# Kernel tuning notes

Measured on AMD Instinct MI355X. Metric: run time of the kernel, lower is better.

The kernel has to match this reference:

```python
import jax, jax.numpy as jnp
import numpy as np

B, S, D, H, W = 2, 4096, 1024, 8, 1024  # batch, seq, model_dim, heads, window
DH = D // H
EPS = 1e-5


def setup_inputs() -> dict:
    key = jax.random.key(0)
    ks = jax.random.split(key, 4)
    scale = 0.02
    return {
        "val": jax.random.normal(ks[0], (B, S, D), dtype=jnp.float32),
        "w_qkv": jax.random.normal(ks[1], (D, 3 * D), dtype=jnp.float32) * scale,
        "b_qkv": jnp.zeros((3 * D,), dtype=jnp.float32),
        "w_out": jax.random.normal(ks[2], (D, D), dtype=jnp.float32) * scale,
        "b_out": jnp.zeros((D,), dtype=jnp.float32),
        "ln_gamma": jnp.ones((D,), dtype=jnp.float32),
        "ln_beta": jnp.zeros((D,), dtype=jnp.float32),
    }


def _layer_norm(x, gamma, beta):
    mu = jnp.mean(x, axis=-1, keepdims=True)
    var = jnp.mean(jnp.square(x - mu), axis=-1, keepdims=True)
    return (x - mu) * jax.lax.rsqrt(var + EPS) * gamma + beta


def reference(val, w_qkv, b_qkv, w_out, b_out, ln_gamma, ln_beta):
    nb = S // W  # number of local windows
    qkv = val @ w_qkv + b_qkv                       # [B, S, 3D]
    qkv = qkv.reshape(B, nb, W, 3, H, DH)
    q, k, v = qkv[..., 0, :, :], qkv[..., 1, :, :], qkv[..., 2, :, :]  # [B,nb,W,H,DH]
    scores = jnp.einsum("bnwhd,bnxhd->bnhwx", q, k) / jnp.sqrt(jnp.float32(DH))
    attn = jax.nn.softmax(scores, axis=-1)          # [B,nb,H,W,W]
    ctx = jnp.einsum("bnhwx,bnxhd->bnwhd", attn, v).reshape(B, S, D)
    attn_out = ctx @ w_out + b_out                  # [B,S,D]
    return _layer_norm(val + attn_out, ln_gamma, ln_beta)
```

## Files before the change

### kernel.cpp

```cpp
#include <hip/hip_runtime.h>
#include <hip/hip_bf16.h>
#include <stdint.h>


typedef float f32x4 __attribute__((ext_vector_type(4)));
typedef __bf16 bf16x8 __attribute__((ext_vector_type(8)));

static __device__ __forceinline__ unsigned short f2bf(float f) {
    unsigned int u = __builtin_bit_cast(unsigned int, f);
    u += 0x7fffu + ((u >> 16) & 1u);
    return (unsigned short)(u >> 16);
}

static __device__ __forceinline__ unsigned cvt_pk_bf16(float lo, float hi) {
    unsigned r;
    asm("v_cvt_pk_bf16_f32 %0, %1, %2" : "=v"(r) : "v"(lo), "v"(hi));
    return r;
}

static __device__ __forceinline__ void gload_lds16(const void* g, void* l) {
    __builtin_amdgcn_global_load_lds(
        (__attribute__((address_space(1))) void*)(g),
        (__attribute__((address_space(3))) void*)(l), 16, 0, 0);
}

#define VMCNT(n) asm volatile("s_waitcnt vmcnt(" #n ")" ::: "memory")
#define SB() __builtin_amdgcn_sched_barrier(0)

__global__ __launch_bounds__(256) void k_convert(const float* __restrict__ in,
                                                 unsigned short* __restrict__ out,
                                                 int n4) {
    int i = blockIdx.x * 256 + threadIdx.x;
    if (i >= n4) return;
    float4 v = ((const float4*)in)[i];
    ushort4 o;
    o.x = f2bf(v.x); o.y = f2bf(v.y); o.z = f2bf(v.z); o.w = f2bf(v.w);
    ((ushort4*)out)[i] = o;
}

__global__ __launch_bounds__(256) void k_transpose(const float* __restrict__ in,
                                                   unsigned short* __restrict__ out,
                                                   int R, int C) {
    __shared__ float tile[64][65];
    const int rt = blockIdx.y * 64, ct = blockIdx.x * 64;
    const int t = threadIdx.x;
#pragma unroll
    for (int i = 0; i < 4; ++i) {
        int fid = i * 256 + t;
        int r = fid >> 4;
        int c = (fid & 15) << 2;
        float4 v = *(const float4*)&in[(size_t)(rt + r) * C + ct + c];
        tile[r][c] = v.x; tile[r][c + 1] = v.y; tile[r][c + 2] = v.z; tile[r][c + 3] = v.w;
    }
    __syncthreads();
#pragma unroll
    for (int i = 0; i < 4; ++i) {
        int fid = i * 256 + t;
        int c = fid >> 4;
        int r0 = (fid & 15) << 2;
        ushort4 o;
        o.x = f2bf(tile[r0][c]);     o.y = f2bf(tile[r0 + 1][c]);
        o.z = f2bf(tile[r0 + 2][c]); o.w = f2bf(tile[r0 + 3][c]);
        *(ushort4*)&out[(size_t)(ct + c) * R + rt + r0] = o;
    }
}

template <int MODE, int NTILES>
__global__ __launch_bounds__(512) void k_gemm(
    const unsigned short* __restrict__ A,
    const unsigned short* __restrict__ Bt,
    const float* __restrict__ bias,
    const float* __restrict__ resid,
    unsigned short* __restrict__ out_qk,
    unsigned short* __restrict__ out_vT,
    float* __restrict__ out_f)
{
    __shared__ __align__(16) char smem[147456];
    const int t = threadIdx.x;
    const int wave = t >> 6, lane = t & 63;
    const int lr = lane & 15, lg = lane >> 4;
    const int wr = wave >> 1, wc = wave & 1;

    const int lid = blockIdx.x;
    const int swz = (lid & 7) * (4 * NTILES) + (lid >> 3);
    const int tile_m = (swz / NTILES) * 256;
    const int tile_n = (swz % NTILES) * 128;

    const int srow = lane >> 3;
    const int sblk = (lane & 7) ^ srow;

    f32x4 acc[4][4];
#pragma unroll
    for (int i = 0; i < 4; ++i)
#pragma unroll
        for (int j = 0; j < 4; ++j)
            acc[i][j] = (f32x4){0.f, 0.f, 0.f, 0.f};

    auto stage2 = [&](int kt, int buf, int h) {
#pragma unroll
        for (int i = 0; i < 2; ++i) {
            int r = h * 128 + i * 64 + wave * 8 + srow;
            int dst = buf * 49152 + h * 16384 + i * 8192 + wave * 1024 + lane * 16;
            gload_lds16(&A[(size_t)(tile_m + r) * 1024 + kt * 64 + sblk * 8], smem + dst);
        }
        int rb = h * 64 + wave * 8 + srow;
        int dstb = buf * 49152 + 32768 + h * 8192 + wave * 1024 + lane * 16;
        gload_lds16(&Bt[(size_t)(tile_n + rb) * 1024 + kt * 64 + sblk * 8], smem + dstb);
    };

    stage2(0, 0, 0); stage2(0, 0, 1);
    stage2(1, 1, 0); stage2(1, 1, 1);

    bf16x8 af[4][2], bf[2][2];

    for (int kt = 0; kt < 16; ++kt) {
        const int buf = kt % 3;
        if (kt == 15) { VMCNT(0); } else { VMCNT(6); }
        SB(); __builtin_amdgcn_s_barrier(); SB();

        const int abase = buf * 49152;
        const int bbase = buf * 49152 + 32768;

#pragma unroll
        for (int mi = 0; mi < 4; ++mi) {
            const int row = wr * 64 + mi * 16 + lr;
#pragma unroll
            for (int kk = 0; kk < 2; ++kk)
                af[mi][kk] = *(const bf16x8*)(smem + abase + row * 128 +
                                (((kk * 4 + lg) ^ (row & 7)) << 4));
        }
#pragma unroll
        for (int ni = 0; ni < 2; ++ni) {
            const int row = wc * 64 + ni * 16 + lr;
#pragma unroll
            for (int kk = 0; kk < 2; ++kk)
                bf[ni][kk] = *(const bf16x8*)(smem + bbase + row * 128 +
                                (((kk * 4 + lg) ^ (row & 7)) << 4));
        }
        if (kt < 14) stage2(kt + 2, (kt + 2) % 3, 0);

        __builtin_amdgcn_s_setprio(1);
#pragma unroll
        for (int kk = 0; kk < 2; ++kk)
#pragma unroll
            for (int mi = 0; mi < 4; ++mi)
#pragma unroll
                for (int ni = 0; ni < 2; ++ni)
                    acc[mi][ni] = __builtin_amdgcn_mfma_f32_16x16x32_bf16(
                        af[mi][kk], bf[ni][kk], acc[mi][ni], 0, 0, 0);
        __builtin_amdgcn_s_setprio(0);

#pragma unroll
        for (int ni = 0; ni < 2; ++ni) {
            const int row = wc * 64 + 32 + ni * 16 + lr;
#pragma unroll
            for (int kk = 0; kk < 2; ++kk)
                bf[ni][kk] = *(const bf16x8*)(smem + bbase + row * 128 +
                                (((kk * 4 + lg) ^ (row & 7)) << 4));
        }
        if (kt < 14) stage2(kt + 2, (kt + 2) % 3, 1);

        __builtin_amdgcn_s_setprio(1);
#pragma unroll
        for (int kk = 0; kk < 2; ++kk)
#pragma unroll
            for (int mi = 0; mi < 4; ++mi)
#pragma unroll
                for (int ni = 0; ni < 2; ++ni)
                    acc[mi][2 + ni] = __builtin_amdgcn_mfma_f32_16x16x32_bf16(
                        af[mi][kk], bf[ni][kk], acc[mi][2 + ni], 0, 0, 0);
        __builtin_amdgcn_s_setprio(0);
    }

#pragma unroll
    for (int J = 0; J < 4; ++J) {
        const int n = tile_n + wc * 64 + J * 16 + lr;
        const float bv = bias[n];
#pragma unroll
        for (int I = 0; I < 4; ++I) {
            const int m0 = tile_m + wr * 64 + I * 16 + lg * 4;
            f32x4 v = acc[I][J];
            if (MODE == 0) {
                if (n < 2048) {
#pragma unroll
                    for (int r = 0; r < 4; ++r)
                        out_qk[(size_t)(m0 + r) * 2048 + n] = f2bf(v[r] + bv);
                } else {
                    int hd = (n - 2048) >> 7;
                    int dd = (n - 2048) & 127;
                    int bn = m0 >> 10;
                    int x0 = m0 & 1023;
                    ushort4 o;
                    o.x = f2bf(v[0] + bv); o.y = f2bf(v[1] + bv);
                    o.z = f2bf(v[2] + bv); o.w = f2bf(v[3] + bv);
                    *(ushort4*)&out_vT[((size_t)(bn * 8 + hd) * 128 + dd) * 1024 + x0] = o;
                }
            } else {
#pragma unroll
                for (int r = 0; r < 4; ++r) {
                    size_t idx = (size_t)(m0 + r) * 1024 + n;
                    out_f[idx] = v[r] + bv + resid[idx];
                }
            }
        }
    }
}

__global__ __launch_bounds__(256, 2) void k_attn(
    const unsigned short* __restrict__ qk,
    const unsigned short* __restrict__ vT,
    unsigned short* __restrict__ ctx)
{
    __shared__ __align__(16) unsigned short Kl[2 * 64 * 128];
    __shared__ __align__(16) unsigned short Vl[2 * 128 * 64];
    __shared__ __align__(16) unsigned short Pl[128 * 64];
    const int t = threadIdx.x;
    const int wave = t >> 6, lane = t & 63;
    const int lr = lane & 15, lg = lane >> 4;

    const int lid = blockIdx.y * gridDim.x + blockIdx.x;
    const int xcd = lid & 7, slot = lid >> 3;
    const int head = xcd * 8 + (slot & 7);
    const int qblk = slot >> 3;

    const int h = head & 7;
    const int tok0 = (head >> 3) * 1024;
    const int qtok = tok0 + qblk * 128 + wave * 32;
    const float cl2 = 0.08838834764831845f * 1.44269504088896f;

    const unsigned short* kbase = &qk[(size_t)tok0 * 2048 + 1024 + h * 128];
    const unsigned short* vhead = &vT[(size_t)head * 128 * 1024];

    auto stage = [&](int x0, int buf) {
        unsigned short* Kb = (unsigned short*)((char*)Kl + buf * 16384);
        unsigned short* Vb = (unsigned short*)((char*)Vl + buf * 16384);
#pragma unroll
        for (int i = 0; i < 4; ++i) {
            int x = i * 16 + wave * 4 + (lane >> 4);
            int ck = (lane & 15) ^ (x & 7);
            gload_lds16(&kbase[(size_t)(x0 + x) * 2048 + ck * 8], &Kb[i * 2048 + wave * 512]);
            int d = i * 32 + wave * 8 + (lane >> 3);
            int cv = (lane & 7) ^ (d & 7);
            gload_lds16(&vhead[(size_t)d * 1024 + x0 + cv * 8], &Vb[i * 2048 + wave * 512]);
        }
    };

    bf16x8 qf[2][4];
#pragma unroll
    for (int nq = 0; nq < 2; ++nq)
#pragma unroll
        for (int kk = 0; kk < 4; ++kk)
            qf[nq][kk] = *(const bf16x8*)&qk[(size_t)(qtok + 16 * nq + lr) * 2048 + h * 128 + kk * 32 + lg * 8];

    f32x4 o[2][8];
#pragma unroll
    for (int a = 0; a < 2; ++a)
#pragma unroll
        for (int b = 0; b < 8; ++b)
            o[a][b] = (f32x4){0.f, 0.f, 0.f, 0.f};
    float m_run[2] = {-3.0e38f, -3.0e38f};
    float l_run[2] = {0.f, 0.f};

    stage(0, 0);

    for (int tile = 0; tile < 16; ++tile) {
        const int kb = (tile & 1) * 16384;
        if (tile < 15) {
            stage((tile + 1) * 64, (tile + 1) & 1);
            VMCNT(8);
        } else {
            VMCNT(0);
        }
        SB(); __builtin_amdgcn_s_barrier(); SB();

        f32x4 s[4][2];
#pragma unroll
        for (int mi = 0; mi < 4; ++mi)
#pragma unroll
            for (int nq = 0; nq < 2; ++nq)
                s[mi][nq] = (f32x4){0.f, 0.f, 0.f, 0.f};
#pragma unroll
        for (int kk = 0; kk < 4; ++kk) {
            bf16x8 kf[4];
#pragma unroll
            for (int mi = 0; mi < 4; ++mi) {
                int row = mi * 16 + lr;
                int byte = (row * 256 + kk * 64 + lg * 16) ^ ((row & 7) << 4);
                kf[mi] = *(const bf16x8*)((const char*)Kl + kb + byte);
            }
            __builtin_amdgcn_s_setprio(1);
#pragma unroll
            for (int mi = 0; mi < 4; ++mi)
#pragma unroll
                for (int nq = 0; nq < 2; ++nq)
                    s[mi][nq] = __builtin_amdgcn_mfma_f32_16x16x32_bf16(kf[mi], qf[nq][kk], s[mi][nq], 0, 0, 0);
            __builtin_amdgcn_s_setprio(0);
        }

        float fac[2];
        bool doresc[2];
#pragma unroll
        for (int nq = 0; nq < 2; ++nq) {
            float mx = -3.0e38f;
#pragma unroll
            for (int mi = 0; mi < 4; ++mi)
#pragma unroll
                for (int r = 0; r < 4; ++r)
                    mx = fmaxf(mx, s[mi][nq][r]);
            mx = fmaxf(mx, __shfl_xor(mx, 16));
            mx = fmaxf(mx, __shfl_xor(mx, 32));
            float mxl = mx * cl2;
            float mr = m_run[nq];
            if (__any(mxl - mr > 8.0f)) {
                float mn = fmaxf(mr, mxl);
                fac[nq] = __builtin_amdgcn_exp2f(mr - mn);
                m_run[nq] = mn;
                doresc[nq] = true;
            } else {
                fac[nq] = 1.0f;
                doresc[nq] = false;
            }
            const float nmn = -m_run[nq];
            float sum = 0.f;
            const int q = wave * 32 + nq * 16 + lr;
#pragma unroll
            for (int mi = 0; mi < 4; ++mi) {
                float p0 = __builtin_amdgcn_exp2f(__builtin_fmaf(s[mi][nq][0], cl2, nmn));
                float p1 = __builtin_amdgcn_exp2f(__builtin_fmaf(s[mi][nq][1], cl2, nmn));
                float p2 = __builtin_amdgcn_exp2f(__builtin_fmaf(s[mi][nq][2], cl2, nmn));
                float p3 = __builtin_amdgcn_exp2f(__builtin_fmaf(s[mi][nq][3], cl2, nmn));
                sum += (p0 + p1) + (p2 + p3);
                uint2 pk;
                pk.x = cvt_pk_bf16(p0, p1);
                pk.y = cvt_pk_bf16(p2, p3);
                int byte = (q * 128 + (mi * 16 + lg * 4) * 2) ^ ((q & 7) << 4);
                *(uint2*)((char*)Pl + byte) = pk;
            }
            sum += __shfl_xor(sum, 16);
            sum += __shfl_xor(sum, 32);
            l_run[nq] = l_run[nq] * fac[nq] + sum;
        }

#pragma unroll
        for (int mo = 0; mo < 2; ++mo)
            if (doresc[mo]) {
#pragma unroll
                for (int r = 0; r < 4; ++r) {
                    int src = (lane & 48) | (lg * 4 + r);
                    float f = __shfl(fac[mo], src);
#pragma unroll
                    for (int nd = 0; nd < 8; ++nd)
                        o[mo][nd][r] *= f;
                }
            }

#pragma unroll
        for (int kk = 0; kk < 2; ++kk) {
            bf16x8 pf[2], vf[8];
#pragma unroll
            for (int mo = 0; mo < 2; ++mo) {
                int q = wave * 32 + mo * 16 + lr;
                int byte = (q * 128 + kk * 64 + lg * 16) ^ ((q & 7) << 4);
                pf[mo] = *(const bf16x8*)((const char*)Pl + byte);
            }
#pragma unroll
            for (int nd = 0; nd < 8; ++nd) {
                int drow = nd * 16 + lr;
                int byte = (drow * 128 + kk * 64 + lg * 16) ^ ((drow & 7) << 4);
                vf[nd] = *(const bf16x8*)((const char*)Vl + kb + byte);
            }
            __builtin_amdgcn_s_setprio(1);
#pragma unroll
            for (int mo = 0; mo < 2; ++mo)
#pragma unroll
                for (int nd = 0; nd < 8; ++nd)
                    o[mo][nd] = __builtin_amdgcn_mfma_f32_16x16x32_bf16(pf[mo], vf[nd], o[mo][nd], 0, 0, 0);
            __builtin_amdgcn_s_setprio(0);
        }
        __builtin_amdgcn_s_barrier(); SB();
    }

#pragma unroll
    for (int mo = 0; mo < 2; ++mo) {
        float rl[4];
#pragma unroll
        for (int r = 0; r < 4; ++r) {
            int src = (lane & 48) | (lg * 4 + r);
            rl[r] = 1.0f / __shfl(l_run[mo], src);
        }
#pragma unroll
        for (int nd = 0; nd < 8; ++nd)
#pragma unroll
            for (int r = 0; r < 4; ++r) {
                int q = qtok + mo * 16 + lg * 4 + r;
                ctx[(size_t)q * 1024 + h * 128 + nd * 16 + lr] = f2bf(o[mo][nd][r] * rl[r]);
            }
    }
}

__global__ __launch_bounds__(256) void k_ln(float* __restrict__ io,
                                            const float* __restrict__ gamma,
                                            const float* __restrict__ beta)
{
    __shared__ float bs[4], bss[4];
    const int row = blockIdx.x;
    const int t = threadIdx.x;
    float4 v = ((const float4*)&io[(size_t)row * 1024])[t];
    float s = (v.x + v.y) + (v.z + v.w);
    float ss = (v.x * v.x + v.y * v.y) + (v.z * v.z + v.w * v.w);
#pragma unroll
    for (int off = 32; off >= 1; off >>= 1) {
        s += __shfl_xor(s, off);
        ss += __shfl_xor(ss, off);
    }
    if ((t & 63) == 0) { bs[t >> 6] = s; bss[t >> 6] = ss; }
    __syncthreads();
    s = (bs[0] + bs[1]) + (bs[2] + bs[3]);
    ss = (bss[0] + bss[1]) + (bss[2] + bss[3]);
    const float mu = s * (1.f / 1024.f);
    const float var = ss * (1.f / 1024.f) - mu * mu;
    const float rs = rsqrtf(var + 1e-5f);
    float4 g = ((const float4*)gamma)[t];
    float4 b = ((const float4*)beta)[t];
    float4 ov;
    ov.x = (v.x - mu) * rs * g.x + b.x;
    ov.y = (v.y - mu) * rs * g.y + b.y;
    ov.z = (v.z - mu) * rs * g.z + b.z;
    ov.w = (v.w - mu) * rs * g.w + b.w;
    ((float4*)&io[(size_t)row * 1024])[t] = ov;
}

extern "C" void kernel_launch(void* const* d_in, const int* in_sizes, int n_in,
                              void* d_out, int out_size, void* d_ws, size_t ws_size,
                              hipStream_t stream)
{
    const float* val   = (const float*)d_in[0];
    const float* w_qkv = (const float*)d_in[1];
    const float* b_qkv = (const float*)d_in[2];
    const float* w_out = (const float*)d_in[3];
    const float* b_out = (const float*)d_in[4];
    const float* ln_g  = (const float*)d_in[5];
    const float* ln_b  = (const float*)d_in[6];
    float* out = (float*)d_out;

    char* ws = (char*)d_ws;
    unsigned short* qk     = (unsigned short*)(ws + 0);
    unsigned short* vTb    = (unsigned short*)(ws + 33554432);
    unsigned short* ctx    = (unsigned short*)(ws + 50331648);
    unsigned short* w_outT = (unsigned short*)(ws + 67108864);
    unsigned short* w_qkvT = (unsigned short*)(ws + 69206016);
    unsigned short* valb   = (unsigned short*)(ws + 75497472);

    k_convert<<<8192, 256, 0, stream>>>(val, valb, 2097152);
    k_transpose<<<dim3(48, 16), 256, 0, stream>>>(w_qkv, w_qkvT, 1024, 3072);
    k_transpose<<<dim3(16, 16), 256, 0, stream>>>(w_out, w_outT, 1024, 1024);
    k_gemm<0, 24><<<768, 512, 0, stream>>>(valb, w_qkvT, b_qkv, nullptr, qk, vTb, nullptr);
    k_attn<<<dim3(8, 64), 256, 0, stream>>>(qk, vTb, ctx);
    k_gemm<1, 8><<<256, 512, 0, stream>>>(ctx, w_outT, b_out, val, nullptr, nullptr, out);
    k_ln<<<8192, 256, 0, stream>>>(out, ln_g, ln_b);
}
```

Baseline: 155.4 us.

## Split QKV GEMM into dedicated kernel with BK=32 triple-buffered smaller LDS

The QKV projection gets its own kernel, which uses a K-step of 32 instead of 64 and a 3-deep LDS ring of 72KB instead of 144KB. It also uses a new XOR swizzle. The smaller LDS footprint should let two 512-thread blocks share a CU, hiding latency across blocks, and the deeper prefetch overlaps global-to-LDS loads with MFMA work. In exchange there are twice as many K iterations, so barrier and issue overhead per FLOP goes up. The output GEMM is unchanged apart from de-templating.

```diff
diff --git a/kernel.cpp b/kernel.cpp
--- a/kernel.cpp
+++ b/kernel.cpp
@@ -65,14 +65,116 @@
     }
 }
 
-template <int MODE, int NTILES>
-__global__ __launch_bounds__(512) void k_gemm(
+__global__ __launch_bounds__(512) void k_gemm1(
+    const unsigned short* __restrict__ A,
+    const unsigned short* __restrict__ Bt,
+    const float* __restrict__ bias,
+    unsigned short* __restrict__ out_qk,
+    unsigned short* __restrict__ out_vT)
+{
+    __shared__ __align__(16) char smem[73728];
+    const int t = threadIdx.x;
+    const int wave = t >> 6, lane = t & 63;
+    const int lr = lane & 15, lg = lane >> 4;
+    const int wr = wave >> 1, wc = wave & 1;
+
+    const int lid = blockIdx.x;
+    const int swz = (lid & 7) * 96 + (lid >> 3);
+    const int tile_m = (swz / 24) * 256;
+    const int tile_n = (swz % 24) * 128;
+
+    const int sr = (lane >> 2);
+    const int sc0 = lane & 3;
+
+    f32x4 acc[4][4];
+#pragma unroll
+    for (int i = 0; i < 4; ++i)
+#pragma unroll
+        for (int j = 0; j < 4; ++j)
+            acc[i][j] = (f32x4){0.f, 0.f, 0.f, 0.f};
+
+    auto stage = [&](int kt, int buf) {
+#pragma unroll
+        for (int i = 0; i < 2; ++i) {
+            int r = i * 128 + wave * 16 + sr;
+            int c = sc0 ^ ((r >> 2) & 3);
+            int dst = buf * 24576 + i * 8192 + wave * 1024 + lane * 16;
+            gload_lds16(&A[(size_t)(tile_m + r) * 1024 + kt * 32 + c * 8], smem + dst);
+        }
+        int rb = wave * 16 + sr;
+        int cb = sc0 ^ ((rb >> 2) & 3);
+        int dstb = buf * 24576 + 16384 + wave * 1024 + lane * 16;
+        gload_lds16(&Bt[(size_t)(tile_n + rb) * 1024 + kt * 32 + cb * 8], smem + dstb);
+    };
+
+    stage(0, 0);
+    stage(1, 1);
+
+    bf16x8 af[4], bf[4];
+
+    for (int kt = 0; kt < 32; ++kt) {
+        const int buf = kt % 3;
+        if (kt == 31) { VMCNT(0); } else { VMCNT(3); }
+        SB(); __builtin_amdgcn_s_barrier(); SB();
+
+        const int abase = buf * 24576;
+        const int bbase = buf * 24576 + 16384;
+
+#pragma unroll
+        for (int mi = 0; mi < 4; ++mi) {
+            const int row = wr * 64 + mi * 16 + lr;
+            af[mi] = *(const bf16x8*)(smem + abase + row * 64 +
+                            ((lg ^ ((row >> 2) & 3)) << 4));
+        }
+#pragma unroll
+        for (int ni = 0; ni < 4; ++ni) {
+            const int row = wc * 64 + ni * 16 + lr;
+            bf[ni] = *(const bf16x8*)(smem + bbase + row * 64 +
+                            ((lg ^ ((row >> 2) & 3)) << 4));
+        }
+        if (kt <= 29) stage(kt + 2, (kt + 2) % 3);
+
+        __builtin_amdgcn_s_setprio(1);
+#pragma unroll
+        for (int mi = 0; mi < 4; ++mi)
+#pragma unroll
+            for (int ni = 0; ni < 4; ++ni)
+                acc[mi][ni] = __builtin_amdgcn_mfma_f32_16x16x32_bf16(
+                    af[mi], bf[ni], acc[mi][ni], 0, 0, 0);
+        __builtin_amdgcn_s_setprio(0);
+    }
+
+#pragma unroll
+    for (int J = 0; J < 4; ++J) {
+        const int n = tile_n + wc * 64 + J * 16 + lr;
+        const float bv = bias[n];
+#pragma unroll
+        for (int I = 0; I < 4; ++I) {
+            const int m0 = tile_m + wr * 64 + I * 16 + lg * 4;
+            f32x4 v = acc[I][J];
+            if (n < 2048) {
+#pragma unroll
+                for (int r = 0; r < 4; ++r)
+                    out_qk[(size_t)(m0 + r) * 2048 + n] = f2bf(v[r] + bv);
+            } else {
+                int hd = (n - 2048) >> 7;
+                int dd = (n - 2048) & 127;
+                int bn = m0 >> 10;
+                int x0 = m0 & 1023;
+                ushort4 o;
+                o.x = f2bf(v[0] + bv); o.y = f2bf(v[1] + bv);
+                o.z = f2bf(v[2] + bv); o.w = f2bf(v[3] + bv);
+                *(ushort4*)&out_vT[((size_t)(bn * 8 + hd) * 128 + dd) * 1024 + x0] = o;
+            }
+        }
+    }
+}
+
+__global__ __launch_bounds__(512) void k_gemm2(
     const unsigned short* __restrict__ A,
     const unsigned short* __restrict__ Bt,
     const float* __restrict__ bias,
     const float* __restrict__ resid,
-    unsigned short* __restrict__ out_qk,
-    unsigned short* __restrict__ out_vT,
     float* __restrict__ out_f)
 {
     __shared__ __align__(16) char smem[147456];
@@ -82,9 +184,9 @@
     const int wr = wave >> 1, wc = wave & 1;
 
     const int lid = blockIdx.x;
-    const int swz = (lid & 7) * (4 * NTILES) + (lid >> 3);
-    const int tile_m = (swz / NTILES) * 256;
-    const int tile_n = (swz % NTILES) * 128;
+    const int swz = (lid & 7) * 32 + (lid >> 3);
+    const int tile_m = (swz / 8) * 256;
+    const int tile_n = (swz % 8) * 128;
 
     const int srow = lane >> 3;
     const int sblk = (lane & 7) ^ srow;
@@ -180,27 +282,10 @@
         for (int I = 0; I < 4; ++I) {
             const int m0 = tile_m + wr * 64 + I * 16 + lg * 4;
             f32x4 v = acc[I][J];
-            if (MODE == 0) {
-                if (n < 2048) {
-#pragma unroll
-                    for (int r = 0; r < 4; ++r)
-                        out_qk[(size_t)(m0 + r) * 2048 + n] = f2bf(v[r] + bv);
-                } else {
-                    int hd = (n - 2048) >> 7;
-                    int dd = (n - 2048) & 127;
-                    int bn = m0 >> 10;
-                    int x0 = m0 & 1023;
-                    ushort4 o;
-                    o.x = f2bf(v[0] + bv); o.y = f2bf(v[1] + bv);
-                    o.z = f2bf(v[2] + bv); o.w = f2bf(v[3] + bv);
-                    *(ushort4*)&out_vT[((size_t)(bn * 8 + hd) * 128 + dd) * 1024 + x0] = o;
-                }
-            } else {
-#pragma unroll
-                for (int r = 0; r < 4; ++r) {
-                    size_t idx = (size_t)(m0 + r) * 1024 + n;
-                    out_f[idx] = v[r] + bv + resid[idx];
-                }
+#pragma unroll
+            for (int r = 0; r < 4; ++r) {
+                size_t idx = (size_t)(m0 + r) * 1024 + n;
+                out_f[idx] = v[r] + bv + resid[idx];
             }
         }
     }
@@ -454,8 +539,8 @@
     k_convert<<<8192, 256, 0, stream>>>(val, valb, 2097152);
     k_transpose<<<dim3(48, 16), 256, 0, stream>>>(w_qkv, w_qkvT, 1024, 3072);
     k_transpose<<<dim3(16, 16), 256, 0, stream>>>(w_out, w_outT, 1024, 1024);
-    k_gemm<0, 24><<<768, 512, 0, stream>>>(valb, w_qkvT, b_qkv, nullptr, qk, vTb, nullptr);
+    k_gemm1<<<768, 512, 0, stream>>>(valb, w_qkvT, b_qkv, qk, vTb);
     k_attn<<<dim3(8, 64), 256, 0, stream>>>(qk, vTb, ctx);
-    k_gemm<1, 8><<<256, 512, 0, stream>>>(ctx, w_outT, b_out, val, nullptr, nullptr, out);
+    k_gemm2<<<256, 512, 0, stream>>>(ctx, w_outT, b_out, val, out);
     k_ln<<<8192, 256, 0, stream>>>(out, ln_g, ln_b);
 }
```

Measured after the change: 160.7 us, median of 4. +3.4%, slower.
